# Kernel optimization log

Measured on AMD Instinct MI355X. Metric: run time of the kernel, lower is better.

The kernel has to match this reference:

```python
import jax, jax.numpy as jnp
import numpy as np

B, N, C, D = 1, 8192, 256, 128
MASK_VAL = jnp.float32(-1e16)


def setup_inputs() -> dict:
    key = jax.random.key(0)
    k_in, k_g, k_w, k_b = jax.random.split(key, 4)
    inputs = jax.random.normal(k_in, (B, N, C), dtype=jnp.float32)
    # row has at least one unmasked entry (standard GAT practice).
    graph = (jax.random.uniform(k_g, (N, N)) < 0.01).astype(jnp.float32)
    graph = jnp.maximum(graph, jnp.eye(N, dtype=jnp.float32))
    W = jax.random.normal(k_w, (D, C), dtype=jnp.float32)  # nn.Linear weight [out,in]
    b = jax.random.normal(k_b, (D,), dtype=jnp.float32)
    return {"inputs": inputs, "graph": graph, "W": W, "b": b}


def reference(inputs, graph, W, b):
    # h = W(inputs): [B,N,D]
    h = jnp.einsum('bnc,dc->bnd', inputs, W)
    # dense scores masked by adjacency: [B,N,N]
    scores = jnp.einsum('bnd,bmd->bnm', h, h) * graph[None, :, :]
    # torch: masked_fill_(scores == 0, -1e16)
    scores = jnp.where(scores == 0.0, MASK_VAL, scores)
    attention = jax.nn.softmax(scores, axis=2)
    return jnp.einsum('bnm,bmd->bnd', attention, h) + b
```

## Files before the change

### kernel.cpp

```cpp
#include <hip/hip_runtime.h>
#include <math.h>

#define Nn 8192
#define Cc 256
#define Dd 128
#define CAP 192

typedef float fx4 __attribute__((ext_vector_type(4)));

__global__ __launch_bounds__(256) void wt_kernel(const float* __restrict__ W,
                                                 float4* __restrict__ WT) {
  const int t = blockIdx.x * 256 + threadIdx.x;
  const int c4 = t >> 7;
  const int d  = t & 127;
  const float4 v = *(const float4*)(W + (size_t)d * Cc + c4 * 4);
  WT[c4 * Dd + d] = v;
}

__global__ __launch_bounds__(256) void h_kernel(const float* __restrict__ x,
                                                const float4* __restrict__ WT,
                                                float* __restrict__ h) {
  const int tid = threadIdx.x;
  const int d = tid & 127;
  const int g = tid >> 7;
  const int r0 = blockIdx.x * 16 + g * 8;
  const float4* x4 = (const float4*)(x + (size_t)r0 * Cc);

  float acc[8];
#pragma unroll
  for (int r = 0; r < 8; ++r) acc[r] = 0.f;

#pragma unroll 4
  for (int c4 = 0; c4 < Cc / 4; ++c4) {
    const float4 w = WT[c4 * Dd + d];
#pragma unroll
    for (int r = 0; r < 8; ++r) {
      const float4 u = x4[r * (Cc / 4) + c4];
      acc[r] += u.x * w.x + u.y * w.y + u.z * w.z + u.w * w.w;
    }
  }
#pragma unroll
  for (int r = 0; r < 8; ++r) {
    h[(size_t)(r0 + r) * Dd + d] = acc[r];
  }
}

#define COMPACT(comp, cidx)                                             \
  {                                                                     \
    const unsigned long long mk = __ballot((comp) != 0.f);              \
    if (mk) {                                                           \
      const int p = cnt + __popcll(mk & lmask);                         \
      if ((comp) != 0.f && p < CAP) idx[p] = col + (cidx);              \
      cnt += __popcll(mk);                                              \
    }                                                                   \
  }

__device__ __forceinline__ void tail_step(int s, int m, const int* idx, int i,
                                          const float* __restrict__ h,
                                          int q, int ql,
                                          const float4& hiA, const float4& hiB,
                                          float& M, float& L,
                                          float4& accA, float4& accB) {
  const int e = s * 4 + q;
  const int j = (e < m) ? idx[e] : i;
  const float4 hvA = *(const float4*)(h + (size_t)j * Dd + ql * 8);
  const float4 hvB = *(const float4*)(h + (size_t)j * Dd + ql * 8 + 4);
  float pd = hiA.x * hvA.x + hiA.y * hvA.y + hiA.z * hvA.z + hiA.w * hvA.w
           + hiB.x * hvB.x + hiB.y * hvB.y + hiB.z * hvB.z + hiB.w * hvB.w;
#pragma unroll
  for (int off = 8; off > 0; off >>= 1) pd += __shfl_xor(pd, off);
  const float sc = (e < m) ? pd : 0.f;
  if (sc != 0.f) {
    const float newM = fmaxf(M, sc);
    const float scale = __expf(M - newM);
    const float p = __expf(sc - newM);
    L = L * scale + p;
    accA.x = accA.x * scale + p * hvA.x;  accA.y = accA.y * scale + p * hvA.y;
    accA.z = accA.z * scale + p * hvA.z;  accA.w = accA.w * scale + p * hvA.w;
    accB.x = accB.x * scale + p * hvB.x;  accB.y = accB.y * scale + p * hvB.y;
    accB.z = accB.z * scale + p * hvB.z;  accB.w = accB.w * scale + p * hvB.w;
    M = newM;
  }
}

__device__ __forceinline__ void merge_write(int i, const float* __restrict__ bias,
                                            float* __restrict__ out, int q, int ql,
                                            float M, float L, float4 accA, float4 accB) {
#pragma unroll
  for (int off = 16; off <= 32; off <<= 1) {
    const float Mo = __shfl_xor(M, off);
    const float Lo = __shfl_xor(L, off);
    float4 aAo, aBo;
    aAo.x = __shfl_xor(accA.x, off); aAo.y = __shfl_xor(accA.y, off);
    aAo.z = __shfl_xor(accA.z, off); aAo.w = __shfl_xor(accA.w, off);
    aBo.x = __shfl_xor(accB.x, off); aBo.y = __shfl_xor(accB.y, off);
    aBo.z = __shfl_xor(accB.z, off); aBo.w = __shfl_xor(accB.w, off);
    const float Mm = fmaxf(M, Mo);
    const float s0 = (M  > -INFINITY) ? __expf(M  - Mm) : 0.f;
    const float s1 = (Mo > -INFINITY) ? __expf(Mo - Mm) : 0.f;
    L = L * s0 + Lo * s1;
    accA.x = accA.x * s0 + aAo.x * s1;  accA.y = accA.y * s0 + aAo.y * s1;
    accA.z = accA.z * s0 + aAo.z * s1;  accA.w = accA.w * s0 + aAo.w * s1;
    accB.x = accB.x * s0 + aBo.x * s1;  accB.y = accB.y * s0 + aBo.y * s1;
    accB.z = accB.z * s0 + aBo.z * s1;  accB.w = accB.w * s0 + aBo.w * s1;
    M = Mm;
  }
  const float inv = 1.f / L;
  if (q == 0) {
    const float4 bA = *(const float4*)(bias + ql * 8);
    const float4 bB = *(const float4*)(bias + ql * 8 + 4);
    float4 oA, oB;
    oA.x = accA.x * inv + bA.x;  oA.y = accA.y * inv + bA.y;
    oA.z = accA.z * inv + bA.z;  oA.w = accA.w * inv + bA.w;
    oB.x = accB.x * inv + bB.x;  oB.y = accB.y * inv + bB.y;
    oB.z = accB.z * inv + bB.z;  oB.w = accB.w * inv + bB.w;
    *(float4*)(out + (size_t)i * Dd + ql * 8)     = oA;
    *(float4*)(out + (size_t)i * Dd + ql * 8 + 4) = oB;
  }
}

__global__ __launch_bounds__(256, 4) void gat_fused(const float* __restrict__ graph,
                                                    const float* __restrict__ h,
                                                    const float* __restrict__ bias,
                                                    float* __restrict__ out) {
  __shared__ int idxs[8][CAP];
  const int wv   = threadIdx.x >> 6;
  const int lane = threadIdx.x & 63;
  const int q    = lane >> 4;
  const int ql   = lane & 15;
  const int iA = blockIdx.x * 8 + wv * 2;
  const int iB = iA + 1;
  int* idxA = idxs[wv * 2];
  int* idxB = idxs[wv * 2 + 1];
  const unsigned long long lmask = (1ull << lane) - 1ull;

  const float4 hiA_A = *(const float4*)(h + (size_t)iA * Dd + ql * 8);
  const float4 hiB_A = *(const float4*)(h + (size_t)iA * Dd + ql * 8 + 4);
  const float4 hiA_B = *(const float4*)(h + (size_t)iB * Dd + ql * 8);
  const float4 hiB_B = *(const float4*)(h + (size_t)iB * Dd + ql * 8 + 4);

  int mA;
  {
    const fx4* row = (const fx4*)(graph + (size_t)iA * Nn);
    int* idx = idxA;
    int cnt = 0;
    fx4 v[8];
#pragma unroll
    for (int t = 0; t < 8; ++t)
      v[t] = __builtin_nontemporal_load(&row[t * 64 + lane]);
#pragma unroll
    for (int c = 0; c < 4; ++c) {
#pragma unroll
      for (int t = 0; t < 8; ++t) {
        const fx4 cur = v[t];
        if (c < 3)
          v[t] = __builtin_nontemporal_load(&row[(c + 1) * 8 * 64 + t * 64 + lane]);
        const int col = 4 * ((c * 8 + t) * 64 + lane);
        COMPACT(cur.x, 0) COMPACT(cur.y, 1) COMPACT(cur.z, 2) COMPACT(cur.w, 3)
      }
    }
    mA = min(cnt, CAP);
  }

  float MA = -INFINITY, LA = 0.f;
  float4 accA_A = {0.f, 0.f, 0.f, 0.f}, accB_A = {0.f, 0.f, 0.f, 0.f};
  int sA = 0;
  const int nsA = (mA + 3) >> 2;

  int mB;
  {
    const fx4* row = (const fx4*)(graph + (size_t)iB * Nn);
    int* idx = idxB;
    int cnt = 0;
    fx4 v[8];
#pragma unroll
    for (int t = 0; t < 8; ++t)
      v[t] = __builtin_nontemporal_load(&row[t * 64 + lane]);
#pragma unroll
    for (int c = 0; c < 4; ++c) {
#pragma unroll
      for (int t = 0; t < 8; ++t) {
        const fx4 cur = v[t];
        if (c < 3)
          v[t] = __builtin_nontemporal_load(&row[(c + 1) * 8 * 64 + t * 64 + lane]);
        const int col = 4 * ((c * 8 + t) * 64 + lane);
        COMPACT(cur.x, 0) COMPACT(cur.y, 1) COMPACT(cur.z, 2) COMPACT(cur.w, 3)
        if (sA < nsA) {
          tail_step(sA, mA, idxA, iA, h, q, ql, hiA_A, hiB_A, MA, LA, accA_A, accB_A);
          ++sA;
        }
      }
    }
    mB = min(cnt, CAP);
  }

  for (; sA < nsA; ++sA)
    tail_step(sA, mA, idxA, iA, h, q, ql, hiA_A, hiB_A, MA, LA, accA_A, accB_A);
  merge_write(iA, bias, out, q, ql, MA, LA, accA_A, accB_A);

  float MB = -INFINITY, LB = 0.f;
  float4 accA_B = {0.f, 0.f, 0.f, 0.f}, accB_B = {0.f, 0.f, 0.f, 0.f};
  const int nsB = (mB + 3) >> 2;
  for (int s = 0; s < nsB; ++s)
    tail_step(s, mB, idxB, iB, h, q, ql, hiA_B, hiB_B, MB, LB, accA_B, accB_B);
  merge_write(iB, bias, out, q, ql, MB, LB, accA_B, accB_B);
}

extern "C" void kernel_launch(void* const* d_in, const int* in_sizes, int n_in,
                              void* d_out, int out_size, void* d_ws, size_t ws_size,
                              hipStream_t stream) {
  const float* x     = (const float*)d_in[0];
  const float* graph = (const float*)d_in[1];
  const float* W     = (const float*)d_in[2];
  const float* bias  = (const float*)d_in[3];
  float* out = (float*)d_out;

  float*  h  = (float*)d_ws;
  float4* WT = (float4*)((char*)d_ws + (16u << 20));

  wt_kernel<<<32, 256, 0, stream>>>(W, WT);
  h_kernel<<<Nn / 16, 256, 0, stream>>>(x, WT, h);
  gat_fused<<<Nn / 8, 256, 0, stream>>>(graph, h, bias, out);
}
```

Baseline: 410.9 us.

## Software-pipeline neighbor gathers and use DPP row reductions for dot products

Splits each tail step into a gather load and a consume phase so the h-row loads for neighbor s+1 are issued before step s is consumed. Row A is pipelined inside the row-B compaction loop and row B is processed in double-buffered pairs, aiming to hide gather latency. The 16-lane shuffle reduction is replaced by DPP row_shr adds, which avoids LDS-based shuffles. The cost is more registers, which may reduce occupancy. The DPP shifts also leave only one lane per 16-lane row (lane 15) holding the full sum, while the score is used in every lane, so the softmax values and results may be wrong.

```diff
diff --git a/kernel.cpp b/kernel.cpp
--- a/kernel.cpp
+++ b/kernel.cpp
@@ -7,6 +7,19 @@
 #define CAP 192
 
 typedef float fx4 __attribute__((ext_vector_type(4)));
+
+template <int CTRL>
+__device__ __forceinline__ float dpp_radd(float x) {
+  const int y = __builtin_amdgcn_update_dpp(0, __float_as_int(x), CTRL, 0xf, 0xf, false);
+  return x + __int_as_float(y);
+}
+__device__ __forceinline__ float quarter_sum(float x) {
+  x = dpp_radd<0x128>(x);
+  x = dpp_radd<0x124>(x);
+  x = dpp_radd<0x122>(x);
+  x = dpp_radd<0x121>(x);
+  return x;
+}
 
 __global__ __launch_bounds__(256) void wt_kernel(const float* __restrict__ W,
                                                  float4* __restrict__ WT) {
@@ -29,7 +42,6 @@
   float acc[8];
 #pragma unroll
   for (int r = 0; r < 8; ++r) acc[r] = 0.f;
-
 #pragma unroll 4
   for (int c4 = 0; c4 < Cc / 4; ++c4) {
     const float4 w = WT[c4 * Dd + d];
@@ -40,9 +52,7 @@
     }
   }
 #pragma unroll
-  for (int r = 0; r < 8; ++r) {
-    h[(size_t)(r0 + r) * Dd + d] = acc[r];
-  }
+  for (int r = 0; r < 8; ++r) h[(size_t)(r0 + r) * Dd + d] = acc[r];
 }
 
 #define COMPACT(comp, cidx)                                             \
@@ -55,20 +65,24 @@
     }                                                                   \
   }
 
-__device__ __forceinline__ void tail_step(int s, int m, const int* idx, int i,
-                                          const float* __restrict__ h,
-                                          int q, int ql,
-                                          const float4& hiA, const float4& hiB,
-                                          float& M, float& L,
-                                          float4& accA, float4& accB) {
+__device__ __forceinline__ void tail_load(int s, int m, const int* idx, int i,
+                                          const float* __restrict__ h, int q, int ql,
+                                          float4& hvA, float4& hvB) {
   const int e = s * 4 + q;
   const int j = (e < m) ? idx[e] : i;
-  const float4 hvA = *(const float4*)(h + (size_t)j * Dd + ql * 8);
-  const float4 hvB = *(const float4*)(h + (size_t)j * Dd + ql * 8 + 4);
+  hvA = *(const float4*)(h + (size_t)j * Dd + ql * 8);
+  hvB = *(const float4*)(h + (size_t)j * Dd + ql * 8 + 4);
+}
+
+__device__ __forceinline__ void tail_consume(int s, int m, int q,
+                                             const float4& hvA, const float4& hvB,
+                                             const float4& hiA, const float4& hiB,
+                                             float& M, float& L,
+                                             float4& accA, float4& accB) {
   float pd = hiA.x * hvA.x + hiA.y * hvA.y + hiA.z * hvA.z + hiA.w * hvA.w
            + hiB.x * hvB.x + hiB.y * hvB.y + hiB.z * hvB.z + hiB.w * hvB.w;
-#pragma unroll
-  for (int off = 8; off > 0; off >>= 1) pd += __shfl_xor(pd, off);
+  pd = quarter_sum(pd);
+  const int e = s * 4 + q;
   const float sc = (e < m) ? pd : 0.f;
   if (sc != 0.f) {
     const float newM = fmaxf(M, sc);
@@ -161,12 +175,11 @@
     }
     mA = min(cnt, CAP);
   }
+  const int nsA = (mA + 3) >> 2;
 
   float MA = -INFINITY, LA = 0.f;
   float4 accA_A = {0.f, 0.f, 0.f, 0.f}, accB_A = {0.f, 0.f, 0.f, 0.f};
-  int sA = 0;
-  const int nsA = (mA + 3) >> 2;
-
+  float4 tA[2], tB[2];
   int mB;
   {
     const fx4* row = (const fx4*)(graph + (size_t)iB * Nn);
@@ -180,29 +193,51 @@
     for (int c = 0; c < 4; ++c) {
 #pragma unroll
       for (int t = 0; t < 8; ++t) {
+        const int it = c * 8 + t;
+        if (it < nsA)
+          tail_load(it, mA, idxA, iA, h, q, ql, tA[it & 1], tB[it & 1]);
         const fx4 cur = v[t];
         if (c < 3)
           v[t] = __builtin_nontemporal_load(&row[(c + 1) * 8 * 64 + t * 64 + lane]);
         const int col = 4 * ((c * 8 + t) * 64 + lane);
         COMPACT(cur.x, 0) COMPACT(cur.y, 1) COMPACT(cur.z, 2) COMPACT(cur.w, 3)
-        if (sA < nsA) {
-          tail_step(sA, mA, idxA, iA, h, q, ql, hiA_A, hiB_A, MA, LA, accA_A, accB_A);
-          ++sA;
-        }
+        if (it >= 1 && (it - 1) < nsA)
+          tail_consume(it - 1, mA, q, tA[(it - 1) & 1], tB[(it - 1) & 1],
+                       hiA_A, hiB_A, MA, LA, accA_A, accB_A);
       }
     }
     mB = min(cnt, CAP);
   }
-
-  for (; sA < nsA; ++sA)
-    tail_step(sA, mA, idxA, iA, h, q, ql, hiA_A, hiB_A, MA, LA, accA_A, accB_A);
+  if (31 < nsA)
+    tail_consume(31, mA, q, tA[31 & 1], tB[31 & 1], hiA_A, hiB_A, MA, LA, accA_A, accB_A);
+  for (int s = 32; s < nsA; ++s) {
+    float4 a, b;
+    tail_load(s, mA, idxA, iA, h, q, ql, a, b);
+    tail_consume(s, mA, q, a, b, hiA_A, hiB_A, MA, LA, accA_A, accB_A);
+  }
   merge_write(iA, bias, out, q, ql, MA, LA, accA_A, accB_A);
 
   float MB = -INFINITY, LB = 0.f;
   float4 accA_B = {0.f, 0.f, 0.f, 0.f}, accB_B = {0.f, 0.f, 0.f, 0.f};
   const int nsB = (mB + 3) >> 2;
-  for (int s = 0; s < nsB; ++s)
-    tail_step(s, mB, idxB, iB, h, q, ql, hiA_B, hiB_B, MB, LB, accA_B, accB_B);
+  float4 uA[2], uB[2];
+#pragma unroll
+  for (int u = 0; u < 2; ++u)
+    tail_load(u, mB, idxB, iB, h, q, ql, uA[u], uB[u]);
+  const int nbb = (nsB + 1) >> 1;
+  for (int b = 0; b < nbb; ++b) {
+    float4 nA[2], nB[2];
+    if (b + 1 < nbb) {
+#pragma unroll
+      for (int u = 0; u < 2; ++u)
+        tail_load((b + 1) * 2 + u, mB, idxB, iB, h, q, ql, nA[u], nB[u]);
+    }
+#pragma unroll
+    for (int u = 0; u < 2; ++u)
+      tail_consume(b * 2 + u, mB, q, uA[u], uB[u], hiA_B, hiB_B, MB, LB, accA_B, accB_B);
+#pragma unroll
+    for (int u = 0; u < 2; ++u) { uA[u] = nA[u]; uB[u] = nB[u]; }
+  }
   merge_write(iB, bias, out, q, ql, MB, LB, accA_B, accB_B);
 }
 
```

Result: no change. 402.9 us (-2.0%).
